# Kernel optimization log

Measured on AMD Instinct MI355X. Metric: run time of the kernel, lower is better.

## Reference

```python
import jax, jax.numpy as jnp
import numpy as np

B, S, OBS, D, H, F, L, A = 64, 512, 128, 512, 8, 2048, 4, 16
KERNEL_EPS = 1e-3  # performer kernel_epsilon
LN_EPS = 1e-6      # flax LayerNorm default


def _layernorm(x, s, b):
    m = jnp.mean(x, axis=-1, keepdims=True)
    v = jnp.mean(jnp.square(x - m), axis=-1, keepdims=True)
    return (x - m) * jax.lax.rsqrt(v + LN_EPS) * s + b


def _favor_attn(x, Wq, bq, Wk, bk, Wv, bv, Wo, bo):
    # FAVOR+ generalized attention, deterministic relu features, bidirectional,
    # renormalize_attention=True. phi(u) = relu(u) + kernel_epsilon.
    Bx, Sx, Dx = x.shape
    hd = Dx // H
    q = (x @ Wq + bq).reshape(Bx, Sx, H, hd)
    k = (x @ Wk + bk).reshape(Bx, Sx, H, hd)
    v = (x @ Wv + bv).reshape(Bx, Sx, H, hd)
    pq = jax.nn.relu(q) + KERNEL_EPS  # [B,S,H,m]
    pk = jax.nn.relu(k) + KERNEL_EPS
    kv = jnp.einsum('bshm,bshd->bhmd', pk, v)      # [B,H,m,hd]
    num = jnp.einsum('bshm,bhmd->bshd', pq, kv)    # [B,S,H,hd]
    ksum = jnp.sum(pk, axis=1)                      # [B,H,m]
    den = jnp.einsum('bshm,bhm->bsh', pq, ksum)    # [B,S,H]
    out = num / den[..., None]
    return out.reshape(Bx, Sx, Dx) @ Wo + bo


def setup_inputs() -> dict:
    key = jax.random.key(0)
    ks = jax.random.split(key, 32)
    sc = lambda *shape: 0.02
    inp = {
        'hidden_state': jax.random.normal(ks[0], (B, 1, D), jnp.float32),
        'ins': jax.random.normal(ks[1], (B, S, OBS), jnp.float32),
        'resets': jax.random.randint(ks[2], (B,), 0, 2) > 0,
        'W_emb': jax.random.normal(ks[3], (OBS, D), jnp.float32) * 0.02,
        'b_emb': jnp.zeros((D,), jnp.float32),
        'Wq': jax.random.normal(ks[4], (L, D, D), jnp.float32) * 0.02,
        'bq': jnp.zeros((L, D), jnp.float32),
        'Wk': jax.random.normal(ks[5], (L, D, D), jnp.float32) * 0.02,
        'bk': jnp.zeros((L, D), jnp.float32),
        'Wv': jax.random.normal(ks[6], (L, D, D), jnp.float32) * 0.02,
        'bv': jnp.zeros((L, D), jnp.float32),
        'Wo': jax.random.normal(ks[7], (L, D, D), jnp.float32) * 0.02,
        'bo': jnp.zeros((L, D), jnp.float32),
        'ln1_s': jnp.ones((L, D), jnp.float32),
        'ln1_b': jnp.zeros((L, D), jnp.float32),
        'ln2_s': jnp.ones((L, D), jnp.float32),
        'ln2_b': jnp.zeros((L, D), jnp.float32),
        'W1': jax.random.normal(ks[8], (L, D, F), jnp.float32) * 0.02,
        'b1': jnp.zeros((L, F), jnp.float32),
        'W2': jax.random.normal(ks[9], (L, F, D), jnp.float32) * 0.02,
        'b2': jnp.zeros((L, D), jnp.float32),
        'W_qp': jax.random.normal(ks[10], (D, A), jnp.float32) * 0.02,
        'b_qp': jnp.zeros((A,), jnp.float32),
    }
    return inp


def reference(hidden_state, ins, resets, W_emb, b_emb, Wq, bq, Wk, bk, Wv, bv,
              Wo, bo, ln1_s, ln1_b, ln2_s, ln2_b, W1, b1, W2, b2, W_qp, b_qp):
    emb = ins @ W_emb + b_emb                                   # [B,S,D]
    h0 = jnp.where(resets[:, None, None], jnp.zeros_like(hidden_state), hidden_state)
    x = jnp.concatenate([h0, emb], axis=1)                      # [B,S+1,D]
    for l in range(Wq.shape[0]):
        att = _favor_attn(x, Wq[l], bq[l], Wk[l], bk[l], Wv[l], bv[l], Wo[l], bo[l])
        x = _layernorm(att + x, ln1_s[l], ln1_b[l])
        ff = jax.nn.relu(x @ W1[l] + b1[l]) @ W2[l] + b2[l]
        x = _layernorm(ff + x, ln2_s[l], ln2_b[l])
    h_out = x[:, 0:1, :]                                        # [B,1,D]
    q_vals = h_out @ W_qp + b_qp                                # [B,1,A]
    return (h_out, q_vals)
```

## Files before the change

### kernel.cpp

```cpp
#include <hip/hip_runtime.h>

typedef __bf16 bf16;
typedef __bf16 bf16x8 __attribute__((ext_vector_type(8)));
typedef float  f32x4  __attribute__((ext_vector_type(4)));


__device__ __forceinline__ void cp16(const bf16* g, bf16* l)
{
    __builtin_amdgcn_global_load_lds(
        (const __attribute__((address_space(1))) void*)g,
        (__attribute__((address_space(3))) void*)l,
        16, 0, 0);
}

__global__ __launch_bounds__(256) void cvt_bf16(
    const float* __restrict__ src, bf16* __restrict__ dst, int n)
{
    for (int i = blockIdx.x * 256 + threadIdx.x; i < n; i += gridDim.x * 256)
        dst[i] = (bf16)src[i];
}

__global__ __launch_bounds__(256) void transpose_f32(
    const float* __restrict__ W, bf16* __restrict__ WT, int K, int N, long elemOff)
{
    __shared__ bf16 tile[32][33];
    const int bn = blockIdx.x * 32;
    const int bk = blockIdx.y * 32;
    const int tx = threadIdx.x & 31, ty = threadIdx.x >> 5;
    for (int r = 0; r < 32; r += 8)
        tile[ty + r][tx] = (bf16)W[elemOff + (long)(bk + ty + r) * N + (bn + tx)];
    __syncthreads();
    for (int r = 0; r < 32; r += 8)
        WT[(long)(bn + ty + r) * K + (bk + tx)] = tile[tx][ty + r];
}

__global__ __launch_bounds__(256) void build_x0(
    const float* __restrict__ hs, const int* __restrict__ resets,
    bf16* __restrict__ xb)
{
    const int b = blockIdx.x;
    const bool rz = (resets[b] != 0);
    const long base = (long)b * 513 * 512;
    for (int d = threadIdx.x; d < 512; d += 256)
        xb[base + d] = rz ? (bf16)0.f : (bf16)hs[b * 512 + d];
}

template<int ROWMAP, int ACT>
__global__ __launch_bounds__(256) void gemm128(
    const bf16* __restrict__ A, const bf16* __restrict__ BT,
    const float* __restrict__ bias, bf16* __restrict__ outB,
    int M, int N, int K)
{
    __shared__ bf16 As[128 * 32];
    __shared__ bf16 Bs[128 * 32];
    const int tid  = threadIdx.x;
    const int wave = tid >> 6;
    const int lane = tid & 63;
    const int q    = lane >> 4;
    const int lm   = lane & 15;
    const int wr   = wave >> 1, wc = wave & 1;
    int m0 = blockIdx.y * 128;
    if (m0 > M - 128) m0 = M - 128;
    const int n0 = blockIdx.x * 128;

    const int r0 = wave * 32 + (lane >> 2);
    const int ks = (lane & 3) * 8;
    const bf16* Ag0 = A  + (long)(m0 + r0) * K + ks;
    const bf16* Ag1 = A  + (long)(m0 + r0 + 16) * K + ks;
    const bf16* Bg0 = BT + (long)(n0 + r0) * K + ks;
    const bf16* Bg1 = BT + (long)(n0 + r0 + 16) * K + ks;
    bf16* Al0 = As + wave * 1024;
    bf16* Al1 = As + wave * 1024 + 512;
    bf16* Bl0 = Bs + wave * 1024;
    bf16* Bl1 = Bs + wave * 1024 + 512;

    f32x4 acc[4][4];
    for (int i = 0; i < 4; i++) for (int j = 0; j < 4; j++)
        for (int r = 0; r < 4; r++) acc[i][j][r] = 0.f;

    for (int k0 = 0; k0 < K; k0 += 32) {
        cp16(Ag0 + k0, Al0);
        cp16(Ag1 + k0, Al1);
        cp16(Bg0 + k0, Bl0);
        cp16(Bg1 + k0, Bl1);
        __syncthreads();
        bf16x8 af[4], bfr[4];
        #pragma unroll
        for (int i = 0; i < 4; i++)
            af[i] = *(const bf16x8*)(As + (wr * 64 + i * 16 + lm) * 32 + q * 8);
        #pragma unroll
        for (int j = 0; j < 4; j++)
            bfr[j] = *(const bf16x8*)(Bs + (wc * 64 + j * 16 + lm) * 32 + q * 8);
        #pragma unroll
        for (int i = 0; i < 4; i++)
            #pragma unroll
            for (int j = 0; j < 4; j++)
                acc[i][j] = __builtin_amdgcn_mfma_f32_16x16x32_bf16(
                    af[i], bfr[j], acc[i][j], 0, 0, 0);
        __syncthreads();
    }

    #pragma unroll
    for (int j = 0; j < 4; j++) {
        const int col = n0 + wc * 64 + j * 16 + lm;
        const float bv = bias[col];
        #pragma unroll
        for (int i = 0; i < 4; i++) {
            #pragma unroll
            for (int r = 0; r < 4; r++) {
                int row = m0 + wr * 64 + i * 16 + q * 4 + r;
                float vv = acc[i][j][r] + bv;
                if (ACT >= 1) vv = fmaxf(vv, 0.f);
                if (ACT == 2) vv += 1e-3f;
                if (ROWMAP == 1) row = row + (row >> 9) + 1;
                outB[(long)row * N + col] = (bf16)vv;
            }
        }
    }
}

#define FP 72
__global__ __launch_bounds__(256) void favor_mfma(
    const bf16* pq, const bf16* __restrict__ pk,
    const bf16* __restrict__ v, bf16* ao)
{
    const int bh = blockIdx.x;
    const int b = bh >> 3, h = bh & 7;
    const long base = ((long)b * 513 * 8 + h) * 64;

    __shared__ bf16 pkT[64][FP];
    __shared__ bf16 vT [64][FP];
    __shared__ bf16 kvT[64][FP];
    __shared__ bf16 pqS[64][FP];
    __shared__ float ksumS[64];
    __shared__ float denS[64];

    const int tid  = threadIdx.x;
    const int wave = tid >> 6;
    const int lane = tid & 63;
    const int q    = lane >> 4;
    const int lm   = lane & 15;
    const int wr   = wave >> 1, wc = wave & 1;
    const int mp   = (tid & 31) * 2;
    const int sr   = tid >> 5;

    if (tid < 64) ksumS[tid] = 0.f;
    float ksp0 = 0.f, ksp1 = 0.f;

    f32x4 akv[2][2];
    for (int i = 0; i < 2; i++) for (int j = 0; j < 2; j++)
        for (int r = 0; r < 4; r++) akv[i][j][r] = 0.f;

    for (int t8 = 0; t8 < 9; t8++) {
        const int s0 = t8 * 64;
        #pragma unroll
        for (int i = 0; i < 8; i++) {
            const int s  = sr + i * 8;
            const int gs = s0 + s;
            unsigned pkw = 0, vw = 0;
            if (gs < 513) {
                pkw = *(const unsigned*)(pk + base + (long)gs * 512 + mp);
                vw  = *(const unsigned*)(v  + base + (long)gs * 512 + mp);
            }
            union { unsigned u; bf16 hh[2]; } pu, vu;
            pu.u = pkw; vu.u = vw;
            pkT[mp][s]     = pu.hh[0];
            pkT[mp + 1][s] = pu.hh[1];
            vT[mp][s]      = vu.hh[0];
            vT[mp + 1][s]  = vu.hh[1];
            ksp0 += (float)pu.hh[0];
            ksp1 += (float)pu.hh[1];
        }
        __syncthreads();
        #pragma unroll
        for (int ks = 0; ks < 2; ks++) {
            bf16x8 a0 = *(const bf16x8*)(&pkT[wr * 32 + lm     ][ks * 32 + q * 8]);
            bf16x8 a1 = *(const bf16x8*)(&pkT[wr * 32 + 16 + lm][ks * 32 + q * 8]);
            bf16x8 b0 = *(const bf16x8*)(&vT [wc * 32 + lm     ][ks * 32 + q * 8]);
            bf16x8 b1 = *(const bf16x8*)(&vT [wc * 32 + 16 + lm][ks * 32 + q * 8]);
            akv[0][0] = __builtin_amdgcn_mfma_f32_16x16x32_bf16(a0, b0, akv[0][0], 0, 0, 0);
            akv[0][1] = __builtin_amdgcn_mfma_f32_16x16x32_bf16(a0, b1, akv[0][1], 0, 0, 0);
            akv[1][0] = __builtin_amdgcn_mfma_f32_16x16x32_bf16(a1, b0, akv[1][0], 0, 0, 0);
            akv[1][1] = __builtin_amdgcn_mfma_f32_16x16x32_bf16(a1, b1, akv[1][1], 0, 0, 0);
        }
        __syncthreads();
    }
    atomicAdd(&ksumS[mp],     ksp0);
    atomicAdd(&ksumS[mp + 1], ksp1);
    #pragma unroll
    for (int i = 0; i < 2; i++)
        #pragma unroll
        for (int j = 0; j < 2; j++)
            #pragma unroll
            for (int r = 0; r < 4; r++)
                kvT[wc * 32 + j * 16 + lm][wr * 32 + i * 16 + q * 4 + r] =
                    (bf16)akv[i][j][r];
    __syncthreads();

    const int prow = tid >> 2;
    const int pseg = (tid & 3) * 16;
    for (int t8 = 0; t8 < 9; t8++) {
        const int s0 = t8 * 64;
        const int gs = s0 + prow;
        if (gs < 513) {
            *(bf16x8*)(&pqS[prow][pseg])     = *(const bf16x8*)(pq + base + (long)gs * 512 + pseg);
            *(bf16x8*)(&pqS[prow][pseg + 8]) = *(const bf16x8*)(pq + base + (long)gs * 512 + pseg + 8);
        } else {
            bf16x8 z;
            for (int r = 0; r < 8; r++) z[r] = (bf16)0.f;
            *(bf16x8*)(&pqS[prow][pseg])     = z;
            *(bf16x8*)(&pqS[prow][pseg + 8]) = z;
        }
        __syncthreads();
        {
            const int s = tid >> 2, mb = (tid & 3) * 16;
            float dp = 0.f;
            #pragma unroll
            for (int m2 = 0; m2 < 16; m2++)
                dp += (float)pqS[s][mb + m2] * ksumS[mb + m2];
            dp += __shfl_xor(dp, 1);
            dp += __shfl_xor(dp, 2);
            if ((tid & 3) == 0) denS[s] = dp;
        }
        __syncthreads();
        f32x4 an[4];
        for (int j = 0; j < 4; j++)
            for (int r = 0; r < 4; r++) an[j][r] = 0.f;
        #pragma unroll
        for (int ks = 0; ks < 2; ks++) {
            bf16x8 a = *(const bf16x8*)(&pqS[wave * 16 + lm][ks * 32 + q * 8]);
            #pragma unroll
            for (int j = 0; j < 4; j++) {
                bf16x8 bb = *(const bf16x8*)(&kvT[j * 16 + lm][ks * 32 + q * 8]);
                an[j] = __builtin_amdgcn_mfma_f32_16x16x32_bf16(a, bb, an[j], 0, 0, 0);
            }
        }
        #pragma unroll
        for (int j = 0; j < 4; j++) {
            #pragma unroll
            for (int r = 0; r < 4; r++) {
                const int sl  = wave * 16 + q * 4 + r;
                const int gs2 = s0 + sl;
                if (gs2 < 513) {
                    const int d = j * 16 + lm;
                    ao[base + (long)gs2 * 512 + d] = (bf16)(an[j][r] / denS[sl]);
                }
            }
        }
        __syncthreads();
    }
}

__global__ __launch_bounds__(256) void ln_res(
    const bf16* __restrict__ y, const float* __restrict__ sc,
    const float* __restrict__ bi, bf16* __restrict__ xb)
{
    const int row  = blockIdx.x * 4 + (threadIdx.x >> 6);
    const int lane = threadIdx.x & 63;
    const bf16* yr = y  + (long)row * 512 + lane * 8;
    bf16*       xr = xb + (long)row * 512 + lane * 8;
    bf16x8 yv = *(const bf16x8*)yr;
    bf16x8 xv = *(const bf16x8*)xr;
    float v[8];
    float sum = 0.f;
    #pragma unroll
    for (int i = 0; i < 8; i++) { v[i] = (float)yv[i] + (float)xv[i]; sum += v[i]; }
    #pragma unroll
    for (int o = 32; o; o >>= 1) sum += __shfl_xor(sum, o);
    const float mean = sum * (1.f / 512.f);
    float vs = 0.f;
    #pragma unroll
    for (int i = 0; i < 8; i++) { float dd = v[i] - mean; vs += dd * dd; }
    #pragma unroll
    for (int o = 32; o; o >>= 1) vs += __shfl_xor(vs, o);
    const float rstd = rsqrtf(vs * (1.f / 512.f) + 1e-6f);
    bf16x8 ov;
    #pragma unroll
    for (int i = 0; i < 8; i++)
        ov[i] = (bf16)((v[i] - mean) * rstd * sc[lane * 8 + i] + bi[lane * 8 + i]);
    *(bf16x8*)xr = ov;
}

__global__ __launch_bounds__(256) void final_head(
    const bf16* __restrict__ xb, const float* __restrict__ Wqp,
    const float* __restrict__ bqp, float* __restrict__ out)
{
    const int b = blockIdx.x;
    const bf16* xr = xb + (long)b * 513 * 512;
    for (int i = threadIdx.x; i < 512; i += 256) out[b * 512 + i] = (float)xr[i];
    const int a = threadIdx.x & 15, g = threadIdx.x >> 4;
    float p = 0.f;
    for (int k = g * 32; k < g * 32 + 32; k++)
        p += (float)xr[k] * Wqp[k * 16 + a];
    __shared__ float red[256];
    red[threadIdx.x] = p;
    __syncthreads();
    if (threadIdx.x < 16) {
        float s = bqp[a];
        for (int g2 = 0; g2 < 16; g2++) s += red[g2 * 16 + a];
        out[64 * 512 + b * 16 + a] = s;
    }
}

extern "C" void kernel_launch(void* const* d_in, const int* in_sizes, int n_in,
                              void* d_out, int out_size, void* d_ws, size_t ws_size,
                              hipStream_t stream)
{
    (void)in_sizes; (void)n_in; (void)out_size; (void)ws_size;
    const float* hs    = (const float*)d_in[0];
    const float* ins   = (const float*)d_in[1];
    const int*   resets= (const int*)d_in[2];
    const float* W_emb = (const float*)d_in[3];
    const float* b_emb = (const float*)d_in[4];
    const float* Wq    = (const float*)d_in[5];
    const float* bq    = (const float*)d_in[6];
    const float* Wk    = (const float*)d_in[7];
    const float* bk    = (const float*)d_in[8];
    const float* Wv    = (const float*)d_in[9];
    const float* bv    = (const float*)d_in[10];
    const float* Wo    = (const float*)d_in[11];
    const float* bo    = (const float*)d_in[12];
    const float* ln1s  = (const float*)d_in[13];
    const float* ln1b  = (const float*)d_in[14];
    const float* ln2s  = (const float*)d_in[15];
    const float* ln2b  = (const float*)d_in[16];
    const float* W1    = (const float*)d_in[17];
    const float* b1    = (const float*)d_in[18];
    const float* W2    = (const float*)d_in[19];
    const float* b2    = (const float*)d_in[20];
    const float* Wqp   = (const float*)d_in[21];
    const float* bqp   = (const float*)d_in[22];
    float* out = (float*)d_out;
    char* ws  = (char*)d_ws;

    bf16* xb = (bf16*)(ws);
    bf16* f  = (bf16*)(ws + 33619968);
    bf16* pq = f;
    bf16* pk = (bf16*)(ws + 67239936);
    bf16* vv = (bf16*)(ws + 100990976);
    bf16* ao = pq;
    bf16* y  = vv;
    bf16* WembT = (bf16*)(ws + 134610944);
    char* LW    = ws + 134742016;
    bf16* insb  = (bf16*)(ws + 141033472);

    const bf16* WqT = (const bf16*)(LW + 0);
    const bf16* WkT = (const bf16*)(LW + 524288);
    const bf16* WvT = (const bf16*)(LW + 1048576);
    const bf16* WoT = (const bf16*)(LW + 1572864);
    const bf16* W1T = (const bf16*)(LW + 2097152);
    const bf16* W2T = (const bf16*)(LW + 4194304);

    cvt_bf16<<<4096, 256, 0, stream>>>(ins, insb, 4194304);
    transpose_f32<<<dim3(16, 4), 256, 0, stream>>>(W_emb, WembT, 128, 512, 0);
    build_x0<<<64, 256, 0, stream>>>(hs, resets, xb);
    gemm128<1, 0><<<dim3(4, 256), 256, 0, stream>>>(
        insb, WembT, b_emb, xb, 32768, 512, 128);

    for (int l = 0; l < 4; l++) {
        const long o512  = (long)l * 262144;
        const long o2048 = (long)l * 1048576;
        transpose_f32<<<dim3(16, 16), 256, 0, stream>>>(Wq, (bf16*)(LW + 0),       512, 512,  o512);
        transpose_f32<<<dim3(16, 16), 256, 0, stream>>>(Wk, (bf16*)(LW + 524288),  512, 512,  o512);
        transpose_f32<<<dim3(16, 16), 256, 0, stream>>>(Wv, (bf16*)(LW + 1048576), 512, 512,  o512);
        transpose_f32<<<dim3(16, 16), 256, 0, stream>>>(Wo, (bf16*)(LW + 1572864), 512, 512,  o512);
        transpose_f32<<<dim3(64, 16), 256, 0, stream>>>(W1, (bf16*)(LW + 2097152), 512, 2048, o2048);
        transpose_f32<<<dim3(16, 64), 256, 0, stream>>>(W2, (bf16*)(LW + 4194304), 2048, 512, o2048);

        gemm128<0, 2><<<dim3(4, 257), 256, 0, stream>>>(
            xb, WqT, bq + l * 512, pq, 32832, 512, 512);
        gemm128<0, 2><<<dim3(4, 257), 256, 0, stream>>>(
            xb, WkT, bk + l * 512, pk, 32832, 512, 512);
        gemm128<0, 0><<<dim3(4, 257), 256, 0, stream>>>(
            xb, WvT, bv + l * 512, vv, 32832, 512, 512);
        favor_mfma<<<512, 256, 0, stream>>>(pq, pk, vv, ao);
        gemm128<0, 0><<<dim3(4, 257), 256, 0, stream>>>(
            ao, WoT, bo + l * 512, y, 32832, 512, 512);
        ln_res<<<8208, 256, 0, stream>>>(y, ln1s + l * 512, ln1b + l * 512, xb);

        const int r0s[2] = {0, 16384};
        const int mcs[2] = {16384, 16448};
        for (int c = 0; c < 2; c++) {
            gemm128<0, 1><<<dim3(16, (mcs[c] + 127) / 128), 256, 0, stream>>>(
                xb + (long)r0s[c] * 512, W1T, b1 + l * 2048, f, mcs[c], 2048, 512);
            gemm128<0, 0><<<dim3(4, (mcs[c] + 127) / 128), 256, 0, stream>>>(
                f, W2T, b2 + l * 512, y + (long)r0s[c] * 512, mcs[c], 512, 2048);
        }
        ln_res<<<8208, 256, 0, stream>>>(y, ln2s + l * 512, ln2b + l * 512, xb);
    }

    final_head<<<64, 256, 0, stream>>>(xb, Wqp, bqp, out);
}
```

Baseline: 2.061 ms.

## Double-buffer LDS tiles in gemm128 to overlap global loads with MFMA

Splits the shared A/B tiles into two buffers and prefetches the tile two steps ahead using direct global-to-LDS loads. Manual vmcnt and lgkmcnt waits with raw barriers replace the per-iteration __syncthreads pair. The goal is to hide global memory latency behind the matrix-core work. This doubles LDS use per block, which may lower occupancy, and relies on hand-written wait counts being correct.

After: 2.115 ms. +2.6%, slower.

```diff
diff --git a/kernel.cpp b/kernel.cpp
--- a/kernel.cpp
+++ b/kernel.cpp
@@ -51,8 +51,8 @@
     const float* __restrict__ bias, bf16* __restrict__ outB,
     int M, int N, int K)
 {
-    __shared__ bf16 As[128 * 32];
-    __shared__ bf16 Bs[128 * 32];
+    __shared__ bf16 As[2][128 * 32];
+    __shared__ bf16 Bs[2][128 * 32];
     const int tid  = threadIdx.x;
     const int wave = tid >> 6;
     const int lane = tid & 63;
@@ -69,36 +69,56 @@
     const bf16* Ag1 = A  + (long)(m0 + r0 + 16) * K + ks;
     const bf16* Bg0 = BT + (long)(n0 + r0) * K + ks;
     const bf16* Bg1 = BT + (long)(n0 + r0 + 16) * K + ks;
-    bf16* Al0 = As + wave * 1024;
-    bf16* Al1 = As + wave * 1024 + 512;
-    bf16* Bl0 = Bs + wave * 1024;
-    bf16* Bl1 = Bs + wave * 1024 + 512;
+    const int lb = wave * 1024;
 
     f32x4 acc[4][4];
     for (int i = 0; i < 4; i++) for (int j = 0; j < 4; j++)
         for (int r = 0; r < 4; r++) acc[i][j][r] = 0.f;
 
-    for (int k0 = 0; k0 < K; k0 += 32) {
-        cp16(Ag0 + k0, Al0);
-        cp16(Ag1 + k0, Al1);
-        cp16(Bg0 + k0, Bl0);
-        cp16(Bg1 + k0, Bl1);
-        __syncthreads();
+    const int NT = K >> 5;
+
+#define STAGE(kt, buf)                                         \
+    do {                                                       \
+        const int _k0 = (kt) * 32;                             \
+        cp16(Ag0 + _k0, &As[(buf)][lb]);                       \
+        cp16(Ag1 + _k0, &As[(buf)][lb + 512]);                 \
+        cp16(Bg0 + _k0, &Bs[(buf)][lb]);                       \
+        cp16(Bg1 + _k0, &Bs[(buf)][lb + 512]);                 \
+    } while (0)
+
+    STAGE(0, 0);
+    STAGE(1, 1);
+    asm volatile("s_waitcnt vmcnt(4)" ::: "memory");
+    __builtin_amdgcn_s_barrier();
+
+    for (int t = 0; t < NT; ++t) {
+        const int cur = t & 1;
         bf16x8 af[4], bfr[4];
         #pragma unroll
         for (int i = 0; i < 4; i++)
-            af[i] = *(const bf16x8*)(As + (wr * 64 + i * 16 + lm) * 32 + q * 8);
+            af[i] = *(const bf16x8*)(&As[cur][(wr * 64 + i * 16 + lm) * 32 + q * 8]);
         #pragma unroll
         for (int j = 0; j < 4; j++)
-            bfr[j] = *(const bf16x8*)(Bs + (wc * 64 + j * 16 + lm) * 32 + q * 8);
+            bfr[j] = *(const bf16x8*)(&Bs[cur][(wc * 64 + j * 16 + lm) * 32 + q * 8]);
         #pragma unroll
         for (int i = 0; i < 4; i++)
             #pragma unroll
             for (int j = 0; j < 4; j++)
                 acc[i][j] = __builtin_amdgcn_mfma_f32_16x16x32_bf16(
                     af[i], bfr[j], acc[i][j], 0, 0, 0);
-        __syncthreads();
-    }
+
+        asm volatile("s_waitcnt lgkmcnt(0)" ::: "memory");
+        __builtin_amdgcn_s_barrier();
+
+        if (t + 2 < NT) {
+            STAGE(t + 2, cur);
+            asm volatile("s_waitcnt vmcnt(4)" ::: "memory");
+        } else {
+            asm volatile("s_waitcnt vmcnt(0)" ::: "memory");
+        }
+        __builtin_amdgcn_s_barrier();
+    }
+#undef STAGE
 
     #pragma unroll
     for (int j = 0; j < 4; j++) {
```

## Fuse Q/K/V projections into one GEMM with interleaved QKV buffer and XCD remap

Applied to the files above, without the earlier changes.

Concatenates the transposed Wq/Wk/Wv weights and their biases so one GEMM with N=1536 produces Q, K and V into an interleaved row buffer. The attention kernel and the output projection now read and write with a 1536 row stride. It also adds an XCD-aware block-index remap in the GEMM for better L2 locality, and rebalances the FFN row chunks. The aim is to read the activation matrix once instead of three times and cut launch count, at the cost of strided accesses and a new per-column activation branch.

Measured after the change: 1.906 ms. 1.08x faster.

```diff
diff --git a/kernel.cpp b/kernel.cpp
--- a/kernel.cpp
+++ b/kernel.cpp
@@ -45,11 +45,21 @@
         xb[base + d] = rz ? (bf16)0.f : (bf16)hs[b * 512 + d];
 }
 
+__global__ __launch_bounds__(256) void concat3(
+    const float* __restrict__ a, const float* __restrict__ b,
+    const float* __restrict__ c, float* __restrict__ d)
+{
+    const int i = blockIdx.x * 256 + threadIdx.x;
+    if (i < 512)       d[i] = a[i];
+    else if (i < 1024) d[i] = b[i - 512];
+    else if (i < 1536) d[i] = c[i - 1024];
+}
+
 template<int ROWMAP, int ACT>
 __global__ __launch_bounds__(256) void gemm128(
     const bf16* __restrict__ A, const bf16* __restrict__ BT,
     const float* __restrict__ bias, bf16* __restrict__ outB,
-    int M, int N, int K)
+    int M, int N, int K, int lda, int ldc)
 {
     __shared__ bf16 As[128 * 32];
     __shared__ bf16 Bs[128 * 32];
@@ -59,14 +69,25 @@
     const int q    = lane >> 4;
     const int lm   = lane & 15;
     const int wr   = wave >> 1, wc = wave & 1;
-    int m0 = blockIdx.y * 128;
+
+    int flat;
+    {
+        const int nwg  = gridDim.x * gridDim.y;
+        const int orig = blockIdx.y * gridDim.x + blockIdx.x;
+        const int qq = nwg >> 3, rr = nwg & 7;
+        const int xcd = orig & 7, idx = orig >> 3;
+        flat = (xcd < rr ? xcd * (qq + 1) : rr * (qq + 1) + (xcd - rr) * qq) + idx;
+    }
+    const int bx = flat % gridDim.x;
+    const int by = flat / gridDim.x;
+    int m0 = by * 128;
     if (m0 > M - 128) m0 = M - 128;
-    const int n0 = blockIdx.x * 128;
+    const int n0 = bx * 128;
 
     const int r0 = wave * 32 + (lane >> 2);
     const int ks = (lane & 3) * 8;
-    const bf16* Ag0 = A  + (long)(m0 + r0) * K + ks;
-    const bf16* Ag1 = A  + (long)(m0 + r0 + 16) * K + ks;
+    const bf16* Ag0 = A  + (long)(m0 + r0) * lda + ks;
+    const bf16* Ag1 = A  + (long)(m0 + r0 + 16) * lda + ks;
     const bf16* Bg0 = BT + (long)(n0 + r0) * K + ks;
     const bf16* Bg1 = BT + (long)(n0 + r0 + 16) * K + ks;
     bf16* Al0 = As + wave * 1024;
@@ -110,23 +131,24 @@
             for (int r = 0; r < 4; r++) {
                 int row = m0 + wr * 64 + i * 16 + q * 4 + r;
                 float vv = acc[i][j][r] + bv;
-                if (ACT >= 1) vv = fmaxf(vv, 0.f);
-                if (ACT == 2) vv += 1e-3f;
+                if (ACT == 1) vv = fmaxf(vv, 0.f);
+                if (ACT == 2) vv = fmaxf(vv, 0.f) + 1e-3f;
+                if (ACT == 3 && col < 1024) vv = fmaxf(vv, 0.f) + 1e-3f;
                 if (ROWMAP == 1) row = row + (row >> 9) + 1;
-                outB[(long)row * N + col] = (bf16)vv;
+                outB[(long)row * ldc + col] = (bf16)vv;
             }
         }
     }
 }
 
 #define FP 72
-__global__ __launch_bounds__(256) void favor_mfma(
-    const bf16* pq, const bf16* __restrict__ pk,
-    const bf16* __restrict__ v, bf16* ao)
+__global__ __launch_bounds__(256) void favor_mfma(bf16* qkv)
 {
     const int bh = blockIdx.x;
     const int b = bh >> 3, h = bh & 7;
-    const long base = ((long)b * 513 * 8 + h) * 64;
+    const long rbQ = (long)b * 513 * 1536 + h * 64;
+    const long rbK = rbQ + 512;
+    const long rbV = rbQ + 1024;
 
     __shared__ bf16 pkT[64][FP];
     __shared__ bf16 vT [64][FP];
@@ -159,8 +181,8 @@
             const int gs = s0 + s;
             unsigned pkw = 0, vw = 0;
             if (gs < 513) {
-                pkw = *(const unsigned*)(pk + base + (long)gs * 512 + mp);
-                vw  = *(const unsigned*)(v  + base + (long)gs * 512 + mp);
+                pkw = *(const unsigned*)(qkv + rbK + (long)gs * 1536 + mp);
+                vw  = *(const unsigned*)(qkv + rbV + (long)gs * 1536 + mp);
             }
             union { unsigned u; bf16 hh[2]; } pu, vu;
             pu.u = pkw; vu.u = vw;
@@ -203,8 +225,8 @@
         const int s0 = t8 * 64;
         const int gs = s0 + prow;
         if (gs < 513) {
-            *(bf16x8*)(&pqS[prow][pseg])     = *(const bf16x8*)(pq + base + (long)gs * 512 + pseg);
-            *(bf16x8*)(&pqS[prow][pseg + 8]) = *(const bf16x8*)(pq + base + (long)gs * 512 + pseg + 8);
+            *(bf16x8*)(&pqS[prow][pseg])     = *(const bf16x8*)(qkv + rbQ + (long)gs * 1536 + pseg);
+            *(bf16x8*)(&pqS[prow][pseg + 8]) = *(const bf16x8*)(qkv + rbQ + (long)gs * 1536 + pseg + 8);
         } else {
             bf16x8 z;
             for (int r = 0; r < 8; r++) z[r] = (bf16)0.f;
@@ -243,7 +265,7 @@
                 const int gs2 = s0 + sl;
                 if (gs2 < 513) {
                     const int d = j * 16 + lm;
-                    ao[base + (long)gs2 * 512 + d] = (bf16)(an[j][r] / denS[sl]);
+                    qkv[rbQ + (long)gs2 * 1536 + d] = (bf16)(an[j][r] / denS[sl]);
                 }
             }
         }
@@ -252,12 +274,12 @@
 }
 
 __global__ __launch_bounds__(256) void ln_res(
-    const bf16* __restrict__ y, const float* __restrict__ sc,
+    const bf16* __restrict__ y, int ldy, const float* __restrict__ sc,
     const float* __restrict__ bi, bf16* __restrict__ xb)
 {
     const int row  = blockIdx.x * 4 + (threadIdx.x >> 6);
     const int lane = threadIdx.x & 63;
-    const bf16* yr = y  + (long)row * 512 + lane * 8;
+    const bf16* yr = y  + (long)row * ldy + lane * 8;
     bf16*       xr = xb + (long)row * 512 + lane * 8;
     bf16x8 yv = *(const bf16x8*)yr;
     bf16x8 xv = *(const bf16x8*)xr;
@@ -333,60 +355,51 @@
     float* out = (float*)d_out;
     char* ws  = (char*)d_ws;
 
-    bf16* xb = (bf16*)(ws);
-    bf16* f  = (bf16*)(ws + 33619968);
-    bf16* pq = f;
-    bf16* pk = (bf16*)(ws + 67239936);
-    bf16* vv = (bf16*)(ws + 100990976);
-    bf16* ao = pq;
-    bf16* y  = vv;
-    bf16* WembT = (bf16*)(ws + 134610944);
-    char* LW    = ws + 134742016;
-    bf16* insb  = (bf16*)(ws + 141033472);
-
-    const bf16* WqT = (const bf16*)(LW + 0);
-    const bf16* WkT = (const bf16*)(LW + 524288);
-    const bf16* WvT = (const bf16*)(LW + 1048576);
-    const bf16* WoT = (const bf16*)(LW + 1572864);
-    const bf16* W1T = (const bf16*)(LW + 2097152);
-    const bf16* W2T = (const bf16*)(LW + 4194304);
+    bf16* xb   = (bf16*)(ws);
+    bf16* qkv  = (bf16*)(ws + 33619968);
+    bf16* f    = qkv;
+    bf16* y2   = (bf16*)(ws + 33619968 + 67239936);
+    bf16* WembT= (bf16*)(ws + 134479872);
+    char* LW   = ws + 134610944;
+    bf16* WqkvT= (bf16*)(LW + 0);
+    bf16* WoT  = (bf16*)(LW + 1572864);
+    bf16* W1T  = (bf16*)(LW + 2097152);
+    bf16* W2T  = (bf16*)(LW + 4194304);
+    float* bqkv= (float*)(LW + 6291456);
+    bf16* insb = (bf16*)(ws + 140908544);
 
     cvt_bf16<<<4096, 256, 0, stream>>>(ins, insb, 4194304);
     transpose_f32<<<dim3(16, 4), 256, 0, stream>>>(W_emb, WembT, 128, 512, 0);
     build_x0<<<64, 256, 0, stream>>>(hs, resets, xb);
     gemm128<1, 0><<<dim3(4, 256), 256, 0, stream>>>(
-        insb, WembT, b_emb, xb, 32768, 512, 128);
+        insb, WembT, b_emb, xb, 32768, 512, 128, 128, 512);
 
     for (int l = 0; l < 4; l++) {
         const long o512  = (long)l * 262144;
         const long o2048 = (long)l * 1048576;
-        transpose_f32<<<dim3(16, 16), 256, 0, stream>>>(Wq, (bf16*)(LW + 0),       512, 512,  o512);
-        transpose_f32<<<dim3(16, 16), 256, 0, stream>>>(Wk, (bf16*)(LW + 524288),  512, 512,  o512);
-        transpose_f32<<<dim3(16, 16), 256, 0, stream>>>(Wv, (bf16*)(LW + 1048576), 512, 512,  o512);
-        transpose_f32<<<dim3(16, 16), 256, 0, stream>>>(Wo, (bf16*)(LW + 1572864), 512, 512,  o512);
-        transpose_f32<<<dim3(64, 16), 256, 0, stream>>>(W1, (bf16*)(LW + 2097152), 512, 2048, o2048);
-        transpose_f32<<<dim3(16, 64), 256, 0, stream>>>(W2, (bf16*)(LW + 4194304), 2048, 512, o2048);
-
-        gemm128<0, 2><<<dim3(4, 257), 256, 0, stream>>>(
-            xb, WqT, bq + l * 512, pq, 32832, 512, 512);
-        gemm128<0, 2><<<dim3(4, 257), 256, 0, stream>>>(
-            xb, WkT, bk + l * 512, pk, 32832, 512, 512);
+        transpose_f32<<<dim3(16, 16), 256, 0, stream>>>(Wq, WqkvT,          512, 512,  o512);
+        transpose_f32<<<dim3(16, 16), 256, 0, stream>>>(Wk, WqkvT + 262144, 512, 512,  o512);
+        transpose_f32<<<dim3(16, 16), 256, 0, stream>>>(Wv, WqkvT + 524288, 512, 512,  o512);
+        transpose_f32<<<dim3(16, 16), 256, 0, stream>>>(Wo, WoT,            512, 512,  o512);
+        transpose_f32<<<dim3(64, 16), 256, 0, stream>>>(W1, W1T,            512, 2048, o2048);
+        transpose_f32<<<dim3(16, 64), 256, 0, stream>>>(W2, W2T,            2048, 512, o2048);
+        concat3<<<6, 256, 0, stream>>>(bq + l * 512, bk + l * 512, bv + l * 512, bqkv);
+
+        gemm128<0, 3><<<dim3(12, 257), 256, 0, stream>>>(
+            xb, WqkvT, bqkv, qkv, 32832, 1536, 512, 512, 1536);
+        favor_mfma<<<512, 256, 0, stream>>>(qkv);
         gemm128<0, 0><<<dim3(4, 257), 256, 0, stream>>>(
-            xb, WvT, bv + l * 512, vv, 32832, 512, 512);
-        favor_mfma<<<512, 256, 0, stream>>>(pq, pk, vv, ao);
-        gemm128<0, 0><<<dim3(4, 257), 256, 0, stream>>>(
-            ao, WoT, bo + l * 512, y, 32832, 512, 512);
-        ln_res<<<8208, 256, 0, stream>>>(y, ln1s + l * 512, ln1b + l * 512, xb);
-
-        const int r0s[2] = {0, 16384};
-        const int mcs[2] = {16384, 16448};
+            qkv, WoT, bo + l * 512, qkv + 512, 32832, 512, 512, 1536, 1536);
+        ln_res<<<8208, 256, 0, stream>>>(qkv + 512, 1536, ln1s + l * 512, ln1b + l * 512, xb);
+
         for (int c = 0; c < 2; c++) {
-            gemm128<0, 1><<<dim3(16, (mcs[c] + 127) / 128), 256, 0, stream>>>(
-                xb + (long)r0s[c] * 512, W1T, b1 + l * 2048, f, mcs[c], 2048, 512);
-            gemm128<0, 0><<<dim3(4, (mcs[c] + 127) / 128), 256, 0, stream>>>(
-                f, W2T, b2 + l * 512, y + (long)r0s[c] * 512, mcs[c], 512, 2048);
-        }
-        ln_res<<<8208, 256, 0, stream>>>(y, ln2s + l * 512, ln2b + l * 512, xb);
+            const long r0 = (long)c * 16416;
+            gemm128<0, 1><<<dim3(16, 129), 256, 0, stream>>>(
+                xb + r0 * 512, W1T, b1 + l * 2048, f, 16416, 2048, 512, 512, 2048);
+            gemm128<0, 0><<<dim3(4, 129), 256, 0, stream>>>(
+                f, W2T, b2 + l * 512, y2 + r0 * 512, 16416, 512, 2048, 2048, 512);
+        }
+        ln_res<<<8208, 256, 0, stream>>>(y2, 512, ln2s + l * 512, ln2b + l * 512, xb);
     }
 
     final_head<<<64, 256, 0, stream>>>(xb, Wqp, bqp, out);
```
